# Performance work log

Measured on AMD Instinct MI355X. Metric: run time of the kernel, lower is better.

## Reference

```python
import jax, jax.numpy as jnp
import numpy as np

D = 2048       # hidden_size
F = 8192       # intermediate_size
R = 16         # flylora_rank
SCALING = 32.0 / R   # alpha / rank = 2.0
GAMMA = 0.1


def _era(x):
    # ERA(x) = GELU_tanh(x) + gamma * softplus(x)
    return jax.nn.gelu(x, approximate=True) + GAMMA * jax.nn.softplus(x)


def setup_inputs() -> dict:
    key = jax.random.key(0)
    ks = jax.random.split(key, 16)
    s = 0.02
    inp = {
        'x': jax.random.normal(ks[0], (4, 2048, D), dtype=jnp.float32),
        # gate FlyLoRA (weights stored [in, out])
        'Wg':  jax.random.normal(ks[1], (D, F), dtype=jnp.float32) * s,
        'bg':  jnp.zeros((F,), jnp.float32),
        'Wgd': jax.random.normal(ks[2], (D, R), dtype=jnp.float32) * s,
        'bgd': jnp.zeros((R,), jnp.float32),
        'Wgu': jax.random.normal(ks[3], (R, F), dtype=jnp.float32) * s,
        'bgu': jnp.zeros((F,), jnp.float32),
        # up FlyLoRA
        'Wu':  jax.random.normal(ks[4], (D, F), dtype=jnp.float32) * s,
        'bu':  jnp.zeros((F,), jnp.float32),
        'Wud': jax.random.normal(ks[5], (D, R), dtype=jnp.float32) * s,
        'bud': jnp.zeros((R,), jnp.float32),
        'Wuu': jax.random.normal(ks[6], (R, F), dtype=jnp.float32) * s,
        'buu': jnp.zeros((F,), jnp.float32),
        # down_proj
        'Wd':  jax.random.normal(ks[7], (F, D), dtype=jnp.float32) * s,
        'bd':  jnp.zeros((D,), jnp.float32),
    }
    return inp


def _flylora(x, W, b, Wdn, bdn, Wup, bup):
    # base(x) + scaling * lora_up(lora_down(x))
    base = jnp.einsum('bsd,df->bsf', x, W) + b
    lora = jnp.einsum('bsr,rf->bsf', jnp.einsum('bsd,dr->bsr', x, Wdn) + bdn, Wup) + bup
    return base + SCALING * lora


def reference(x, Wg, bg, Wgd, bgd, Wgu, bgu, Wu, bu, Wud, bud, Wuu, buu, Wd, bd):
    gate = _era(_flylora(x, Wg, bg, Wgd, bgd, Wgu, bgu))
    up = _flylora(x, Wu, bu, Wud, bud, Wuu, buu)
    return jnp.einsum('bsf,fd->bsd', gate * up, Wd) + bd
```

## Files before the change

### kernel.cpp

```cpp
#include <hip/hip_runtime.h>
#include <cstdint>
#include <cstddef>

#define D_DIM 2048
#define F_DIM 8192
#define M_DIM 8192
#define SCALING 2.0f
#define GAMMA 0.1f
#define BUFE 4096

typedef __bf16 bf16x8 __attribute__((ext_vector_type(8)));
typedef float f32x4 __attribute__((ext_vector_type(4)));
typedef unsigned short ushort_t;

__device__ __forceinline__ unsigned short f2bf(float f) {
  unsigned int u = __float_as_uint(f);
  u += 0x7FFF + ((u >> 16) & 1);
  return (unsigned short)(u >> 16);
}

__device__ __forceinline__ float era_f(float x) {
  float x3 = x * x * x;
  float inner = 0.7978845608028654f * (x + 0.044715f * x3);
  float e = __expf(2.0f * inner);
  float th = 1.0f - 2.0f / (e + 1.0f);
  float gelu = 0.5f * x * (1.0f + th);
  float sp = fmaxf(x, 0.0f) + __logf(1.0f + __expf(-fabsf(x)));
  return gelu + GAMMA * sp;
}


__global__ void convert_x(const float* __restrict__ in, ushort_t* __restrict__ out, int n) {
  int i = (blockIdx.x * 256 + threadIdx.x) * 4;
  if (i >= n) return;
  float4 v = *(const float4*)(in + i);
  out[i + 0] = f2bf(v.x);
  out[i + 1] = f2bf(v.y);
  out[i + 2] = f2bf(v.z);
  out[i + 3] = f2bf(v.w);
}

__global__ void transpose_w(const float* __restrict__ in, ushort_t* __restrict__ out,
                            int K, int N) {
  __shared__ float tile[32][33];
  int k0 = blockIdx.y * 32, n0 = blockIdx.x * 32;
  int tr = threadIdx.x >> 5, tc = threadIdx.x & 31;
#pragma unroll
  for (int i = 0; i < 32; i += 8)
    tile[tr + i][tc] = in[(size_t)(k0 + tr + i) * N + n0 + tc];
  __syncthreads();
#pragma unroll
  for (int i = 0; i < 32; i += 8)
    out[(size_t)(n0 + tr + i) * K + k0 + tc] = f2bf(tile[tc][tr + i]);
}

__global__ void pad_small(const float* __restrict__ in, ushort_t* __restrict__ out, int F) {
  int idx = blockIdx.x * 256 + threadIdx.x;
  int f = idx >> 5, k = idx & 31;
  float v = (k < 16) ? in[(size_t)k * F + f] : 0.0f;
  out[idx] = f2bf(v);
}

__global__ void lora_down(const float* __restrict__ x,
                          const float* __restrict__ Wgd, const float* __restrict__ bgd,
                          const float* __restrict__ Wud, const float* __restrict__ bud,
                          ushort_t* __restrict__ xdg, ushort_t* __restrict__ xdu) {
  int row = blockIdx.x * 8 + (threadIdx.x >> 5);
  int c = threadIdx.x & 31;
  bool isG = (c < 16);
  int col = c & 15;
  const float* W = isG ? Wgd : Wud;
  const float* xr = x + (size_t)row * D_DIM;
  float acc = 0.0f;
  for (int k = 0; k < D_DIM; ++k)
    acc = fmaf(xr[k], W[k * 16 + col], acc);
  float b = isG ? bgd[col] : bud[col];
  ushort_t v = f2bf(SCALING * (acc + b));
  ushort_t* dst = isG ? xdg : xdu;
  dst[row * 32 + col] = v;
  dst[row * 32 + 16 + col] = 0;
}


__device__ __forceinline__ void gload16(const ushort_t* g, ushort_t* l) {
  __builtin_amdgcn_global_load_lds(
      (__attribute__((address_space(1))) void*)g,
      (__attribute__((address_space(3))) void*)l, 16, 0, 0);
}

__device__ __forceinline__ bf16x8 frag_ld(const ushort_t* p) {
  union { uint4 u; bf16x8 v; } un;
  un.u = *(const uint4*)p;
  return un.v;
}


__global__ __launch_bounds__(256, 2) void gemm_gateup(
    const ushort_t* __restrict__ xbf, const ushort_t* __restrict__ Wgt,
    const ushort_t* __restrict__ Wut, const ushort_t* __restrict__ Wgup,
    const ushort_t* __restrict__ Wuup, const ushort_t* __restrict__ xdg,
    const ushort_t* __restrict__ xdu,
    const float* __restrict__ bg, const float* __restrict__ bgu,
    const float* __restrict__ bu, const float* __restrict__ buu,
    ushort_t* __restrict__ tout) {
  __shared__ __align__(16) ushort_t xs[2 * BUFE];
  __shared__ __align__(16) ushort_t wgs[2 * BUFE];
  __shared__ __align__(16) ushort_t wus[2 * BUFE];
  const int f0 = blockIdx.x * 128;
  const int m0 = blockIdx.y * 128;
  const int t = threadIdx.x;
  const int w = t >> 6, lane = t & 63;
  const int wm = w >> 1, wn = w & 1;
  const int ml = lane & 15, q = lane >> 4;

  const int srow = t >> 2;
  const int csw = ((t & 3) ^ ((srow >> 1) & 3)) * 8;
  const int slotq = (q ^ ((ml >> 1) & 3)) * 8;
  const int dsto = w * 512;

  unsigned int xoff = (unsigned int)(m0 + srow) * D_DIM + csw;
  unsigned int woff = (unsigned int)(f0 + srow) * D_DIM + csw;
  const unsigned int rstep = 64u * D_DIM;
  const unsigned int lmo = (unsigned int)(m0 + srow) * 32 + csw;
  const unsigned int lfo = (unsigned int)(f0 + srow) * 32 + csw;

  auto stage_main = [&](int cur, unsigned int xo, unsigned int wo) {
    ushort_t* xd = xs + cur * BUFE + dsto;
    ushort_t* gd = wgs + cur * BUFE + dsto;
    ushort_t* ud = wus + cur * BUFE + dsto;
    gload16(xbf + xo, xd);  gload16(xbf + xo + rstep, xd + 2048);
    gload16(Wgt + wo, gd);  gload16(Wgt + wo + rstep, gd + 2048);
    gload16(Wut + wo, ud);  gload16(Wut + wo + rstep, ud + 2048);
  };
  auto stage_lora_g = [&](int cur) {
    ushort_t* xd = xs + cur * BUFE + dsto;
    ushort_t* gd = wgs + cur * BUFE + dsto;
    gload16(xdg + lmo, xd);   gload16(xdg + lmo + 2048, xd + 2048);
    gload16(Wgup + lfo, gd);  gload16(Wgup + lfo + 2048, gd + 2048);
  };
  auto stage_lora_u = [&](int cur) {
    ushort_t* xd = xs + cur * BUFE + dsto;
    ushort_t* ud = wus + cur * BUFE + dsto;
    gload16(xdu + lmo, xd);   gload16(xdu + lmo + 2048, xd + 2048);
    gload16(Wuup + lfo, ud);  gload16(Wuup + lfo + 2048, ud + 2048);
  };

  const f32x4 zero4 = {0.f, 0.f, 0.f, 0.f};
  f32x4 accg[4][4], accu[4][4];
#pragma unroll
  for (int i = 0; i < 4; ++i)
#pragma unroll
    for (int j = 0; j < 4; ++j) { accg[i][j] = zero4; accu[i][j] = zero4; }

  stage_main(0, xoff, woff);

  const int NT = D_DIM / 32;
  for (int kt = 0; kt < NT; ++kt) {
    const int cur = kt & 1;
    xoff += 32; woff += 32;
    __syncthreads();
    if (kt < NT - 1) stage_main(cur ^ 1, xoff, woff);
    else             stage_lora_g(cur ^ 1);

    const ushort_t* xb = xs + cur * BUFE;
    const ushort_t* gb = wgs + cur * BUFE;
    const ushort_t* ub = wus + cur * BUFE;
    bf16x8 af[4], bwf[4];
#pragma unroll
    for (int i = 0; i < 4; ++i) {
      af[i]  = frag_ld(xb + (wm * 64 + i * 16 + ml) * 32 + slotq);
      bwf[i] = frag_ld(gb + (wn * 64 + i * 16 + ml) * 32 + slotq);
    }
#pragma unroll
    for (int mi = 0; mi < 4; ++mi)
#pragma unroll
      for (int ni = 0; ni < 4; ++ni)
        accg[mi][ni] = __builtin_amdgcn_mfma_f32_16x16x32_bf16(af[mi], bwf[ni], accg[mi][ni], 0, 0, 0);
#pragma unroll
    for (int i = 0; i < 4; ++i)
      bwf[i] = frag_ld(ub + (wn * 64 + i * 16 + ml) * 32 + slotq);
#pragma unroll
    for (int mi = 0; mi < 4; ++mi)
#pragma unroll
      for (int ni = 0; ni < 4; ++ni)
        accu[mi][ni] = __builtin_amdgcn_mfma_f32_16x16x32_bf16(af[mi], bwf[ni], accu[mi][ni], 0, 0, 0);
  }

  __syncthreads();
  stage_lora_u(1);
  {
    bf16x8 af[4], bwf[4];
#pragma unroll
    for (int i = 0; i < 4; ++i) {
      af[i]  = frag_ld(xs  + (wm * 64 + i * 16 + ml) * 32 + slotq);
      bwf[i] = frag_ld(wgs + (wn * 64 + i * 16 + ml) * 32 + slotq);
    }
#pragma unroll
    for (int mi = 0; mi < 4; ++mi)
#pragma unroll
      for (int ni = 0; ni < 4; ++ni)
        accg[mi][ni] = __builtin_amdgcn_mfma_f32_16x16x32_bf16(af[mi], bwf[ni], accg[mi][ni], 0, 0, 0);
  }
  __syncthreads();
  {
    bf16x8 af[4], bwf[4];
#pragma unroll
    for (int i = 0; i < 4; ++i) {
      af[i]  = frag_ld(xs  + BUFE + (wm * 64 + i * 16 + ml) * 32 + slotq);
      bwf[i] = frag_ld(wus + BUFE + (wn * 64 + i * 16 + ml) * 32 + slotq);
    }
#pragma unroll
    for (int mi = 0; mi < 4; ++mi)
#pragma unroll
      for (int ni = 0; ni < 4; ++ni)
        accu[mi][ni] = __builtin_amdgcn_mfma_f32_16x16x32_bf16(af[mi], bwf[ni], accu[mi][ni], 0, 0, 0);
  }

#pragma unroll
  for (int ni = 0; ni < 4; ++ni) {
    int col = f0 + wn * 64 + ni * 16 + ml;
    float cbg = bg[col] + SCALING * bgu[col];
    float cbu = bu[col] + SCALING * buu[col];
#pragma unroll
    for (int mi = 0; mi < 4; ++mi) {
      int row0 = m0 + wm * 64 + mi * 16 + q * 4;
#pragma unroll
      for (int r = 0; r < 4; ++r) {
        float hg = accg[mi][ni][r] + cbg;
        float hu = accu[mi][ni][r] + cbu;
        tout[(size_t)(row0 + r) * F_DIM + col] = f2bf(era_f(hg) * hu);
      }
    }
  }
}

__global__ __launch_bounds__(256, 2) void gemm_down(
    const ushort_t* __restrict__ tin, const ushort_t* __restrict__ Wdt,
    const float* __restrict__ bd, float* __restrict__ out) {
  __shared__ __align__(16) ushort_t as_[2 * BUFE];
  __shared__ __align__(16) ushort_t bs_[2 * BUFE];
  const int n0 = blockIdx.x * 128;
  const int m0 = blockIdx.y * 128;
  const int t = threadIdx.x;
  const int w = t >> 6, lane = t & 63;
  const int wm = w >> 1, wn = w & 1;
  const int ml = lane & 15, q = lane >> 4;

  const int srow = t >> 2;
  const int csw = ((t & 3) ^ ((srow >> 1) & 3)) * 8;
  const int slotq = (q ^ ((ml >> 1) & 3)) * 8;
  const int dsto = w * 512;

  unsigned int aoff = (unsigned int)(m0 + srow) * F_DIM + csw;
  unsigned int boff = (unsigned int)(n0 + srow) * F_DIM + csw;
  const unsigned int rstep = 64u * F_DIM;

  auto stage = [&](int cur, unsigned int ao, unsigned int bo) {
    ushort_t* ad = as_ + cur * BUFE + dsto;
    ushort_t* bdst = bs_ + cur * BUFE + dsto;
    gload16(tin + ao, ad);   gload16(tin + ao + rstep, ad + 2048);
    gload16(Wdt + bo, bdst); gload16(Wdt + bo + rstep, bdst + 2048);
  };

  const f32x4 zero4 = {0.f, 0.f, 0.f, 0.f};
  f32x4 acc[4][4];
#pragma unroll
  for (int i = 0; i < 4; ++i)
#pragma unroll
    for (int j = 0; j < 4; ++j) acc[i][j] = zero4;

  stage(0, aoff, boff);

  const int NT = F_DIM / 32;
  for (int kt = 0; kt < NT; ++kt) {
    const int cur = kt & 1;
    aoff += 32; boff += 32;
    __syncthreads();
    if (kt < NT - 1) stage(cur ^ 1, aoff, boff);

    const ushort_t* ab = as_ + cur * BUFE;
    const ushort_t* bb = bs_ + cur * BUFE;
    bf16x8 af[4], bf_[4];
#pragma unroll
    for (int i = 0; i < 4; ++i) {
      af[i]  = frag_ld(ab + (wm * 64 + i * 16 + ml) * 32 + slotq);
      bf_[i] = frag_ld(bb + (wn * 64 + i * 16 + ml) * 32 + slotq);
    }
#pragma unroll
    for (int mi = 0; mi < 4; ++mi)
#pragma unroll
      for (int ni = 0; ni < 4; ++ni)
        acc[mi][ni] = __builtin_amdgcn_mfma_f32_16x16x32_bf16(af[mi], bf_[ni], acc[mi][ni], 0, 0, 0);
  }

#pragma unroll
  for (int ni = 0; ni < 4; ++ni) {
    int col = n0 + wn * 64 + ni * 16 + ml;
    float b = bd[col];
#pragma unroll
    for (int mi = 0; mi < 4; ++mi) {
      int row0 = m0 + wm * 64 + mi * 16 + q * 4;
#pragma unroll
      for (int r = 0; r < 4; ++r)
        out[(size_t)(row0 + r) * D_DIM + col] = acc[mi][ni][r] + b;
    }
  }
}


extern "C" void kernel_launch(void* const* d_in, const int* in_sizes, int n_in,
                              void* d_out, int out_size, void* d_ws, size_t ws_size,
                              hipStream_t stream) {
  const float* x   = (const float*)d_in[0];
  const float* Wg  = (const float*)d_in[1];
  const float* bg  = (const float*)d_in[2];
  const float* Wgd = (const float*)d_in[3];
  const float* bgd = (const float*)d_in[4];
  const float* Wgu = (const float*)d_in[5];
  const float* bgu = (const float*)d_in[6];
  const float* Wu  = (const float*)d_in[7];
  const float* bu  = (const float*)d_in[8];
  const float* Wud = (const float*)d_in[9];
  const float* bud = (const float*)d_in[10];
  const float* Wuu = (const float*)d_in[11];
  const float* buu = (const float*)d_in[12];
  const float* Wd  = (const float*)d_in[13];
  const float* bd  = (const float*)d_in[14];
  float* out = (float*)d_out;

  char* ws = (char*)d_ws;
  size_t off = 0;
  auto alloc = [&](size_t bytes) {
    char* p = ws + off;
    off += (bytes + 255) & ~(size_t)255;
    return p;
  };
  ushort_t* xbf  = (ushort_t*)alloc((size_t)M_DIM * D_DIM * 2);
  ushort_t* Wgt  = (ushort_t*)alloc((size_t)F_DIM * D_DIM * 2);
  ushort_t* Wut  = (ushort_t*)alloc((size_t)F_DIM * D_DIM * 2);
  ushort_t* Wdt  = (ushort_t*)alloc((size_t)D_DIM * F_DIM * 2);
  ushort_t* Wgup = (ushort_t*)alloc((size_t)F_DIM * 32 * 2);
  ushort_t* Wuup = (ushort_t*)alloc((size_t)F_DIM * 32 * 2);
  ushort_t* xdg  = (ushort_t*)alloc((size_t)M_DIM * 32 * 2);
  ushort_t* xdu  = (ushort_t*)alloc((size_t)M_DIM * 32 * 2);
  ushort_t* tbuf = (ushort_t*)alloc((size_t)M_DIM * F_DIM * 2);

  convert_x<<<(M_DIM * D_DIM / 4 + 255) / 256, 256, 0, stream>>>(x, xbf, M_DIM * D_DIM);
  transpose_w<<<dim3(F_DIM / 32, D_DIM / 32), 256, 0, stream>>>(Wg, Wgt, D_DIM, F_DIM);
  transpose_w<<<dim3(F_DIM / 32, D_DIM / 32), 256, 0, stream>>>(Wu, Wut, D_DIM, F_DIM);
  transpose_w<<<dim3(D_DIM / 32, F_DIM / 32), 256, 0, stream>>>(Wd, Wdt, F_DIM, D_DIM);
  pad_small<<<F_DIM * 32 / 256, 256, 0, stream>>>(Wgu, Wgup, F_DIM);
  pad_small<<<F_DIM * 32 / 256, 256, 0, stream>>>(Wuu, Wuup, F_DIM);
  lora_down<<<M_DIM / 8, 256, 0, stream>>>(x, Wgd, bgd, Wud, bud, xdg, xdu);
  gemm_gateup<<<dim3(F_DIM / 128, M_DIM / 128), 256, 0, stream>>>(
      xbf, Wgt, Wut, Wgup, Wuup, xdg, xdu, bg, bgu, bu, buu, tbuf);
  gemm_down<<<dim3(D_DIM / 128, M_DIM / 128), 256, 0, stream>>>(tbuf, Wdt, bd, out);
}
```

Baseline: 1.458 ms.

## Triple-buffer LDS tiles with vmcnt-based waits in both GEMM kernels

Moves both GEMM kernels from double-buffered LDS staging with __syncthreads to a three-stage ring buffer. Each stage waits on partial vmcnt counts before a raw s_barrier, so two tiles of global-to-LDS loads stay in flight while the current tile is computed. This is meant to hide global memory latency behind MFMA work. In exchange it uses 1.5x the LDS, which can limit occupancy under launch_bounds(256,2), and the hand-counted vmcnt values must match the number of loads issued per stage.

```diff
diff --git a/kernel.cpp b/kernel.cpp
--- a/kernel.cpp
+++ b/kernel.cpp
@@ -12,6 +12,8 @@
 typedef __bf16 bf16x8 __attribute__((ext_vector_type(8)));
 typedef float f32x4 __attribute__((ext_vector_type(4)));
 typedef unsigned short ushort_t;
+
+#define VMCNT(n) asm volatile("s_waitcnt vmcnt(" #n ")" ::: "memory")
 
 __device__ __forceinline__ unsigned short f2bf(float f) {
   unsigned int u = __float_as_uint(f);
@@ -103,9 +105,9 @@
     const float* __restrict__ bg, const float* __restrict__ bgu,
     const float* __restrict__ bu, const float* __restrict__ buu,
     ushort_t* __restrict__ tout) {
-  __shared__ __align__(16) ushort_t xs[2 * BUFE];
-  __shared__ __align__(16) ushort_t wgs[2 * BUFE];
-  __shared__ __align__(16) ushort_t wus[2 * BUFE];
+  __shared__ __align__(16) ushort_t xs[3 * BUFE];
+  __shared__ __align__(16) ushort_t wgs[3 * BUFE];
+  __shared__ __align__(16) ushort_t wus[3 * BUFE];
   const int f0 = blockIdx.x * 128;
   const int m0 = blockIdx.y * 128;
   const int t = threadIdx.x;
@@ -124,23 +126,23 @@
   const unsigned int lmo = (unsigned int)(m0 + srow) * 32 + csw;
   const unsigned int lfo = (unsigned int)(f0 + srow) * 32 + csw;
 
-  auto stage_main = [&](int cur, unsigned int xo, unsigned int wo) {
-    ushort_t* xd = xs + cur * BUFE + dsto;
-    ushort_t* gd = wgs + cur * BUFE + dsto;
-    ushort_t* ud = wus + cur * BUFE + dsto;
+  auto stage_main = [&](int bi, unsigned int xo, unsigned int wo) {
+    ushort_t* xd = xs + bi * BUFE + dsto;
+    ushort_t* gd = wgs + bi * BUFE + dsto;
+    ushort_t* ud = wus + bi * BUFE + dsto;
     gload16(xbf + xo, xd);  gload16(xbf + xo + rstep, xd + 2048);
     gload16(Wgt + wo, gd);  gload16(Wgt + wo + rstep, gd + 2048);
     gload16(Wut + wo, ud);  gload16(Wut + wo + rstep, ud + 2048);
   };
-  auto stage_lora_g = [&](int cur) {
-    ushort_t* xd = xs + cur * BUFE + dsto;
-    ushort_t* gd = wgs + cur * BUFE + dsto;
+  auto stage_lora_g = [&](int bi) {
+    ushort_t* xd = xs + bi * BUFE + dsto;
+    ushort_t* gd = wgs + bi * BUFE + dsto;
     gload16(xdg + lmo, xd);   gload16(xdg + lmo + 2048, xd + 2048);
     gload16(Wgup + lfo, gd);  gload16(Wgup + lfo + 2048, gd + 2048);
   };
-  auto stage_lora_u = [&](int cur) {
-    ushort_t* xd = xs + cur * BUFE + dsto;
-    ushort_t* ud = wus + cur * BUFE + dsto;
+  auto stage_lora_u = [&](int bi) {
+    ushort_t* xd = xs + bi * BUFE + dsto;
+    ushort_t* ud = wus + bi * BUFE + dsto;
     gload16(xdu + lmo, xd);   gload16(xdu + lmo + 2048, xd + 2048);
     gload16(Wuup + lfo, ud);  gload16(Wuup + lfo + 2048, ud + 2048);
   };
@@ -152,19 +154,10 @@
 #pragma unroll
     for (int j = 0; j < 4; ++j) { accg[i][j] = zero4; accu[i][j] = zero4; }
 
-  stage_main(0, xoff, woff);
-
-  const int NT = D_DIM / 32;
-  for (int kt = 0; kt < NT; ++kt) {
-    const int cur = kt & 1;
-    xoff += 32; woff += 32;
-    __syncthreads();
-    if (kt < NT - 1) stage_main(cur ^ 1, xoff, woff);
-    else             stage_lora_g(cur ^ 1);
-
-    const ushort_t* xb = xs + cur * BUFE;
-    const ushort_t* gb = wgs + cur * BUFE;
-    const ushort_t* ub = wus + cur * BUFE;
+  auto compute_main = [&](int bi) {
+    const ushort_t* xb = xs + bi * BUFE;
+    const ushort_t* gb = wgs + bi * BUFE;
+    const ushort_t* ub = wus + bi * BUFE;
     bf16x8 af[4], bwf[4];
 #pragma unroll
     for (int i = 0; i < 4; ++i) {
@@ -184,37 +177,63 @@
 #pragma unroll
       for (int ni = 0; ni < 4; ++ni)
         accu[mi][ni] = __builtin_amdgcn_mfma_f32_16x16x32_bf16(af[mi], bwf[ni], accu[mi][ni], 0, 0, 0);
+  };
+  auto compute_lora_g = [&](int bi) {
+    bf16x8 af[4], bwf[4];
+#pragma unroll
+    for (int i = 0; i < 4; ++i) {
+      af[i]  = frag_ld(xs  + bi * BUFE + (wm * 64 + i * 16 + ml) * 32 + slotq);
+      bwf[i] = frag_ld(wgs + bi * BUFE + (wn * 64 + i * 16 + ml) * 32 + slotq);
+    }
+#pragma unroll
+    for (int mi = 0; mi < 4; ++mi)
+#pragma unroll
+      for (int ni = 0; ni < 4; ++ni)
+        accg[mi][ni] = __builtin_amdgcn_mfma_f32_16x16x32_bf16(af[mi], bwf[ni], accg[mi][ni], 0, 0, 0);
+  };
+  auto compute_lora_u = [&](int bi) {
+    bf16x8 af[4], bwf[4];
+#pragma unroll
+    for (int i = 0; i < 4; ++i) {
+      af[i]  = frag_ld(xs  + bi * BUFE + (wm * 64 + i * 16 + ml) * 32 + slotq);
+      bwf[i] = frag_ld(wus + bi * BUFE + (wn * 64 + i * 16 + ml) * 32 + slotq);
+    }
+#pragma unroll
+    for (int mi = 0; mi < 4; ++mi)
+#pragma unroll
+      for (int ni = 0; ni < 4; ++ni)
+        accu[mi][ni] = __builtin_amdgcn_mfma_f32_16x16x32_bf16(af[mi], bwf[ni], accu[mi][ni], 0, 0, 0);
+  };
+
+  stage_main(0, xoff, woff);
+  stage_main(1, xoff + 32, woff + 32);
+  unsigned int xo_n = xoff + 64, wo_n = woff + 64;
+
+  int bc = 0, bs = 2;
+#pragma unroll 1
+  for (int kt = 0; kt < 62; ++kt) {
+    VMCNT(6);
+    __builtin_amdgcn_s_barrier();
+    stage_main(bs, xo_n, wo_n);
+    xo_n += 32; wo_n += 32;
+    compute_main(bc);
+    bc = (bc == 2) ? 0 : bc + 1;
+    bs = (bs == 2) ? 0 : bs + 1;
   }
-
-  __syncthreads();
-  stage_lora_u(1);
-  {
-    bf16x8 af[4], bwf[4];
-#pragma unroll
-    for (int i = 0; i < 4; ++i) {
-      af[i]  = frag_ld(xs  + (wm * 64 + i * 16 + ml) * 32 + slotq);
-      bwf[i] = frag_ld(wgs + (wn * 64 + i * 16 + ml) * 32 + slotq);
-    }
-#pragma unroll
-    for (int mi = 0; mi < 4; ++mi)
-#pragma unroll
-      for (int ni = 0; ni < 4; ++ni)
-        accg[mi][ni] = __builtin_amdgcn_mfma_f32_16x16x32_bf16(af[mi], bwf[ni], accg[mi][ni], 0, 0, 0);
-  }
-  __syncthreads();
-  {
-    bf16x8 af[4], bwf[4];
-#pragma unroll
-    for (int i = 0; i < 4; ++i) {
-      af[i]  = frag_ld(xs  + BUFE + (wm * 64 + i * 16 + ml) * 32 + slotq);
-      bwf[i] = frag_ld(wus + BUFE + (wn * 64 + i * 16 + ml) * 32 + slotq);
-    }
-#pragma unroll
-    for (int mi = 0; mi < 4; ++mi)
-#pragma unroll
-      for (int ni = 0; ni < 4; ++ni)
-        accu[mi][ni] = __builtin_amdgcn_mfma_f32_16x16x32_bf16(af[mi], bwf[ni], accu[mi][ni], 0, 0, 0);
-  }
+  VMCNT(6);
+  __builtin_amdgcn_s_barrier();
+  stage_lora_g(1);
+  compute_main(2);
+  VMCNT(4);
+  __builtin_amdgcn_s_barrier();
+  stage_lora_u(2);
+  compute_main(0);
+  VMCNT(4);
+  __builtin_amdgcn_s_barrier();
+  compute_lora_g(1);
+  VMCNT(0);
+  __builtin_amdgcn_s_barrier();
+  compute_lora_u(2);
 
 #pragma unroll
   for (int ni = 0; ni < 4; ++ni) {
@@ -237,8 +256,8 @@
 __global__ __launch_bounds__(256, 2) void gemm_down(
     const ushort_t* __restrict__ tin, const ushort_t* __restrict__ Wdt,
     const float* __restrict__ bd, float* __restrict__ out) {
-  __shared__ __align__(16) ushort_t as_[2 * BUFE];
-  __shared__ __align__(16) ushort_t bs_[2 * BUFE];
+  __shared__ __align__(16) ushort_t as_[3 * BUFE];
+  __shared__ __align__(16) ushort_t bs_[3 * BUFE];
   const int n0 = blockIdx.x * 128;
   const int m0 = blockIdx.y * 128;
   const int t = threadIdx.x;
@@ -255,9 +274,9 @@
   unsigned int boff = (unsigned int)(n0 + srow) * F_DIM + csw;
   const unsigned int rstep = 64u * F_DIM;
 
-  auto stage = [&](int cur, unsigned int ao, unsigned int bo) {
-    ushort_t* ad = as_ + cur * BUFE + dsto;
-    ushort_t* bdst = bs_ + cur * BUFE + dsto;
+  auto stage = [&](int bi, unsigned int ao, unsigned int bo) {
+    ushort_t* ad = as_ + bi * BUFE + dsto;
+    ushort_t* bdst = bs_ + bi * BUFE + dsto;
     gload16(tin + ao, ad);   gload16(tin + ao + rstep, ad + 2048);
     gload16(Wdt + bo, bdst); gload16(Wdt + bo + rstep, bdst + 2048);
   };
@@ -269,17 +288,9 @@
 #pragma unroll
     for (int j = 0; j < 4; ++j) acc[i][j] = zero4;
 
-  stage(0, aoff, boff);
-
-  const int NT = F_DIM / 32;
-  for (int kt = 0; kt < NT; ++kt) {
-    const int cur = kt & 1;
-    aoff += 32; boff += 32;
-    __syncthreads();
-    if (kt < NT - 1) stage(cur ^ 1, aoff, boff);
-
-    const ushort_t* ab = as_ + cur * BUFE;
-    const ushort_t* bb = bs_ + cur * BUFE;
+  auto compute = [&](int bi) {
+    const ushort_t* ab = as_ + bi * BUFE;
+    const ushort_t* bb = bs_ + bi * BUFE;
     bf16x8 af[4], bf_[4];
 #pragma unroll
     for (int i = 0; i < 4; ++i) {
@@ -291,7 +302,30 @@
 #pragma unroll
       for (int ni = 0; ni < 4; ++ni)
         acc[mi][ni] = __builtin_amdgcn_mfma_f32_16x16x32_bf16(af[mi], bf_[ni], acc[mi][ni], 0, 0, 0);
+  };
+
+  stage(0, aoff, boff);
+  stage(1, aoff + 32, boff + 32);
+  unsigned int ao_n = aoff + 64, bo_n = boff + 64;
+
+  const int NT = F_DIM / 32;
+  int bc = 0, bsn = 2;
+#pragma unroll 1
+  for (int kt = 0; kt < NT - 2; ++kt) {
+    VMCNT(4);
+    __builtin_amdgcn_s_barrier();
+    stage(bsn, ao_n, bo_n);
+    ao_n += 32; bo_n += 32;
+    compute(bc);
+    bc = (bc == 2) ? 0 : bc + 1;
+    bsn = (bsn == 2) ? 0 : bsn + 1;
   }
+  VMCNT(4);
+  __builtin_amdgcn_s_barrier();
+  compute(2);
+  VMCNT(0);
+  __builtin_amdgcn_s_barrier();
+  compute(0);
 
 #pragma unroll
   for (int ni = 0; ni < 4; ++ni) {
```

Result: no change. 1.458 ms (-0.0%).
